# Kernel tuning notes

Hardware: AMD Instinct MI355X
Metric: run time of the kernel (lower is better)

Reference implementation:

```python
import jax, jax.numpy as jnp
import numpy as np

PAD = 20
MAX_DISP = 20
STRIDE2 = 2


def setup_inputs() -> dict:
    key = jax.random.key(0)
    k1, k2 = jax.random.split(key)
    B, C, H, W = 8, 256, 96, 128
    input1 = jax.random.normal(k1, (B, C, H, W), dtype=jnp.float32)
    input2 = jax.random.normal(k2, (B, C, H, W), dtype=jnp.float32)
    return {"input1": input1, "input2": input2}


def reference(input1, input2):
    B, C, H, W = input1.shape
    # zero-pad f2 spatially by PAD on all sides, as ZeroPad2d(pad_size)
    f2pad = jnp.pad(input2, ((0, 0), (0, 0), (PAD, PAD), (PAD, PAD)))
    # displacement offsets: range(i, i + 2*max_disp + 1, stride2) -> 21 per axis
    offs = jnp.arange(0, 2 * MAX_DISP + 1, STRIDE2)
    dy, dx = jnp.meshgrid(offs, offs, indexing="ij")  # h-major flatten matches torch flatten(-2,-1)
    dydx = jnp.stack([dy.ravel(), dx.ravel()], axis=-1)  # [441, 2]

    def step(_, d):
        # shifted view of f2pad: window element (dy, dx) for every pixel (i, j)
        win = jax.lax.dynamic_slice(f2pad, (0, 0, d[0], d[1]), (B, C, H, W))
        # per-pixel inner product over channels
        return None, jnp.einsum("bchw,bchw->bhw", input1, win)

    _, out = jax.lax.scan(step, None, dydx)  # [441, B, H, W]
    out = jnp.transpose(out, (1, 0, 2, 3))  # [B, 441, H, W]
    return out / C
```

## Files before the change

kernel.cpp:

```cpp
#include <hip/hip_runtime.h>
#include <hip/hip_bf16.h>


#define NB 8
#define NC 256
#define NH 96
#define NW 128
#define NU 64
#define ND 21
#define NK 441

typedef __attribute__((ext_vector_type(8))) short s16x8;
typedef __attribute__((ext_vector_type(4))) float f32x4;

__device__ __forceinline__ unsigned short f2bf(float f) {
    unsigned int x = __float_as_uint(f);
    x += 0x7fffu + ((x >> 16) & 1u);
    return (unsigned short)(x >> 16);
}

__global__ __launch_bounds__(256) void repack_kernel(
    const float* __restrict__ in1, const float* __restrict__ in2,
    unsigned short* __restrict__ xg, unsigned short* __restrict__ yg)
{
    int bid = blockIdx.x;
    int src = bid & 1;
    int ct  = (bid >> 1) & 3;
    int rest = bid >> 3;
    int i = rest % NH;
    int b = rest / NH;
    const float* in = src ? in2 : in1;
    unsigned short* og = src ? yg : xg;
    int c0 = ct * 64;

    __shared__ unsigned short tbuf[128][68];

    int tid = threadIdx.x;
    int j  = tid & 127;
    int ch = tid >> 7;
    #pragma unroll 4
    for (int p = 0; p < 32; ++p) {
        int cl = p * 2 + ch;
        float v = in[(((size_t)b * NC + (c0 + cl)) * NH + i) * NW + j];
        tbuf[j][cl] = f2bf(v);
    }
    __syncthreads();
    int c2 = tid & 31;
    int jr = tid >> 5;
    #pragma unroll
    for (int jj0 = 0; jj0 < 128; jj0 += 8) {
        int jj = jj0 + jr;
        int pj = jj & 1, u = jj >> 1;
        unsigned int val = *reinterpret_cast<const unsigned int*>(&tbuf[jj][2 * c2]);
        size_t o = ((((size_t)b * 2 + pj) * NH + i) * NU + u) * NC + c0 + 2 * c2;
        *reinterpret_cast<unsigned int*>(&og[o]) = val;
    }
}

#define XOFF 0
#define YOFF 65536
#define GOFF 131072
#define GPITCH 50
#define ZOFF (GOFF + 2 * 4 * 16 * GPITCH * 4)
#define LDSZ (ZOFF + 16)

__global__ __launch_bounds__(512) void corr_kernel(
    const unsigned short* __restrict__ xg,
    const unsigned short* __restrict__ yg,
    float* __restrict__ out)
{
    __shared__ __align__(16) unsigned char LDS[LDSZ];

    int bid = blockIdx.x;
    int i = bid % NH;
    int b = bid / NH;
    int tid = threadIdx.x;
    int lane = tid & 63;
    int wv = tid >> 6;
    int pj = wv >> 2;
    int tt = wv & 3;

    if (tid == 0) {
        uint4 z = {0u, 0u, 0u, 0u};
        *reinterpret_cast<uint4*>(&LDS[ZOFF]) = z;
    }

    {
        const uint4* src = reinterpret_cast<const uint4*>(xg);
        #pragma unroll
        for (int it = 0; it < 8; ++it) {
            int g = it * 512 + tid;
            int p = g >> 11;
            int rem = g & 2047;
            int u = rem >> 5, off = rem & 31;
            uint4 v = src[(((size_t)(b * 2 + p) * NH + i) * NU + u) * 32 + off];
            int lb = XOFF + (p << 15) + ((u * 512 + off * 16) ^ ((u & 7) << 4));
            *reinterpret_cast<uint4*>(&LDS[lb]) = v;
        }
    }

    const int m  = lane & 15;
    const int kq = lane >> 4;
    const int u  = tt * 16 + m;
    const int xrow = XOFF + (pj << 15) + u * 512;
    const int xsw  = (u & 7) << 4;

    int yb0, yb1, yb2, sw0, sw1, sw2;
    {
        int w0 = tt * 16 - 10 + m;
        int w1 = w0 + 16;
        int w2 = w0 + 32;
        yb0 = (w0 >= 0 && w0 < NU) ? (YOFF + (pj << 15) + w0 * 512) : -1;
        yb1 = (w1 >= 0 && w1 < NU) ? (YOFF + (pj << 15) + w1 * 512) : -1;
        yb2 = (w2 >= 0 && w2 < NU) ? (YOFF + (pj << 15) + w2 * 512) : -1;
        sw0 = (w0 & 7) << 4;
        sw1 = (w1 & 7) << 4;
        sw2 = (w2 & 7) << 4;
    }

    const float inv = 1.0f / 256.0f;

    for (int ky = 0; ky < ND; ++ky) {
        int r = i + 2 * ky - 20;
        bool valid = (r >= 0) && (r < NH);
        size_t obase = (((size_t)b * NK + 21 * ky) * NH + i) * NW + (tid & 127);

        if (valid) {
            const uint4* src = reinterpret_cast<const uint4*>(yg);
            #pragma unroll
            for (int it = 0; it < 8; ++it) {
                int g = it * 512 + tid;
                int p = g >> 11;
                int rem = g & 2047;
                int uu = rem >> 5, off = rem & 31;
                uint4 v = src[(((size_t)(b * 2 + p) * NH + r) * NU + uu) * 32 + off];
                int lb = YOFF + (p << 15) + ((uu * 512 + off * 16) ^ ((uu & 7) << 4));
                *reinterpret_cast<uint4*>(&LDS[lb]) = v;
            }
            __syncthreads();

            f32x4 acc0 = {0.f, 0.f, 0.f, 0.f};
            f32x4 acc1 = {0.f, 0.f, 0.f, 0.f};
            f32x4 acc2 = {0.f, 0.f, 0.f, 0.f};
            #pragma unroll
            for (int ks = 0; ks < 8; ++ks) {
                int c2 = (ks * 32 + kq * 8) * 2;
                s16x8 af = *reinterpret_cast<const s16x8*>(&LDS[xrow + (c2 ^ xsw)]);
                int a0 = (yb0 < 0) ? ZOFF : (yb0 + (c2 ^ sw0));
                s16x8 bf0 = *reinterpret_cast<const s16x8*>(&LDS[a0]);
                acc0 = __builtin_amdgcn_mfma_f32_16x16x32_bf16(af, bf0, acc0, 0, 0, 0);
                int a1 = (yb1 < 0) ? ZOFF : (yb1 + (c2 ^ sw1));
                s16x8 bf1 = *reinterpret_cast<const s16x8*>(&LDS[a1]);
                acc1 = __builtin_amdgcn_mfma_f32_16x16x32_bf16(af, bf1, acc1, 0, 0, 0);
                int a2 = (yb2 < 0) ? ZOFF : (yb2 + (c2 ^ sw2));
                s16x8 bf2 = *reinterpret_cast<const s16x8*>(&LDS[a2]);
                acc2 = __builtin_amdgcn_mfma_f32_16x16x32_bf16(af, bf2, acc2, 0, 0, 0);
            }

            int gb = GOFF + wv * (16 * GPITCH * 4);
            #pragma unroll
            for (int v4 = 0; v4 < 4; ++v4) {
                float* gr = reinterpret_cast<float*>(&LDS[gb + (kq * 4 + v4) * (GPITCH * 4)]);
                gr[m]      = acc0[v4];
                gr[16 + m] = acc1[v4];
                gr[32 + m] = acc2[v4];
            }
            __syncthreads();

            int j = tid & 127;
            int uo = j >> 1;
            int mo = uo & 15;
            const float* grow = reinterpret_cast<const float*>(
                &LDS[GOFF + (((j & 1) * 4 + (uo >> 4)) * 16 + mo) * (GPITCH * 4)]);
            for (int kx = tid >> 7; kx < ND; kx += 4) {
                out[obase + (size_t)kx * (NH * NW)] = grow[mo + kx] * inv;
            }
        } else {
            for (int kx = tid >> 7; kx < ND; kx += 4) {
                out[obase + (size_t)kx * (NH * NW)] = 0.0f;
            }
        }
    }
}

__global__ __launch_bounds__(256) void corr_naive(
    const float* __restrict__ in1, const float* __restrict__ in2, float* __restrict__ out)
{
    size_t o = (size_t)blockIdx.x * 256 + threadIdx.x;
    if (o >= (size_t)NB * NK * NH * NW) return;
    int j = o & 127;
    int i = (int)((o >> 7) % NH);
    size_t rest = o / ((size_t)NH * NW);
    int k = (int)(rest % NK);
    int b = (int)(rest / NK);
    int ky = k / ND, kx = k % ND;
    int r = i + 2 * ky - 20, jc = j + 2 * kx - 20;
    float s = 0.f;
    if (r >= 0 && r < NH && jc >= 0 && jc < NW) {
        const float* p1 = in1 + (((size_t)b * NC) * NH + i) * NW + j;
        const float* p2 = in2 + (((size_t)b * NC) * NH + r) * NW + jc;
        for (int c = 0; c < NC; ++c) { s += p1[0] * p2[0]; p1 += NH * NW; p2 += NH * NW; }
    }
    out[o] = s * (1.0f / 256.0f);
}

extern "C" void kernel_launch(void* const* d_in, const int* in_sizes, int n_in,
                              void* d_out, int out_size, void* d_ws, size_t ws_size,
                              hipStream_t stream) {
    const float* in1 = (const float*)d_in[0];
    const float* in2 = (const float*)d_in[1];
    float* out = (float*)d_out;

    const size_t elems_per_input = (size_t)NB * 2 * NH * NU * NC;
    const size_t need = 2 * elems_per_input * sizeof(unsigned short);

    if (ws_size < need) {
        size_t total = (size_t)NB * NK * NH * NW;
        corr_naive<<<(int)((total + 255) / 256), 256, 0, stream>>>(in1, in2, out);
        return;
    }

    unsigned short* xg = (unsigned short*)d_ws;
    unsigned short* yg = xg + elems_per_input;

    repack_kernel<<<NB * NH * 4 * 2, 256, 0, stream>>>(in1, in2, xg, yg);
    corr_kernel<<<NB * NH, 512, 0, stream>>>(xg, yg, out);
}
```

Before: 230.1 us.

## Load input1 directly into MFMA registers, use 32x32 MFMA, prefetch next row

The repack now covers only input2. The correlation kernel reads input1 straight from global memory, converts it to bf16, and holds it in registers as A fragments, which removes the xg workspace and its LDS staging. The compute moves to 32x32x16 MFMA tiles, and the next input2 row is loaded into registers while the current one is being computed, giving a double-buffered load. Fully padded rows are written as zeros up front, and the block-to-(b,i) mapping is reordered. The costs are higher register pressure (16 A fragments plus 8 staging vectors under launch_bounds 512,2) and strided fp32 reads of input1.

```diff
diff --git a/kernel.cpp b/kernel.cpp
--- a/kernel.cpp
+++ b/kernel.cpp
@@ -9,9 +9,10 @@
 #define NU 64
 #define ND 21
 #define NK 441
+#define HW (NH * NW)
 
 typedef __attribute__((ext_vector_type(8))) short s16x8;
-typedef __attribute__((ext_vector_type(4))) float f32x4;
+typedef __attribute__((ext_vector_type(16))) float f32x16;
 
 __device__ __forceinline__ unsigned short f2bf(float f) {
     unsigned int x = __float_as_uint(f);
@@ -19,30 +20,25 @@
     return (unsigned short)(x >> 16);
 }
 
-__global__ __launch_bounds__(256) void repack_kernel(
-    const float* __restrict__ in1, const float* __restrict__ in2,
-    unsigned short* __restrict__ xg, unsigned short* __restrict__ yg)
+__global__ __launch_bounds__(256) void repack3(
+    const float* __restrict__ in2, unsigned short* __restrict__ yg)
 {
     int bid = blockIdx.x;
-    int src = bid & 1;
-    int ct  = (bid >> 1) & 3;
-    int rest = bid >> 3;
-    int i = rest % NH;
+    int ct = bid & 3;
+    int rest = bid >> 2;
+    int r = rest % NH;
     int b = rest / NH;
-    const float* in = src ? in2 : in1;
-    unsigned short* og = src ? yg : xg;
     int c0 = ct * 64;
 
     __shared__ unsigned short tbuf[128][68];
 
     int tid = threadIdx.x;
-    int j  = tid & 127;
+    int j = tid & 127;
     int ch = tid >> 7;
     #pragma unroll 4
     for (int p = 0; p < 32; ++p) {
         int cl = p * 2 + ch;
-        float v = in[(((size_t)b * NC + (c0 + cl)) * NH + i) * NW + j];
-        tbuf[j][cl] = f2bf(v);
+        tbuf[j][cl] = f2bf(in2[(((size_t)b * NC + (c0 + cl)) * NH + r) * NW + j]);
     }
     __syncthreads();
     int c2 = tid & 31;
@@ -52,133 +48,148 @@
         int jj = jj0 + jr;
         int pj = jj & 1, u = jj >> 1;
         unsigned int val = *reinterpret_cast<const unsigned int*>(&tbuf[jj][2 * c2]);
-        size_t o = ((((size_t)b * 2 + pj) * NH + i) * NU + u) * NC + c0 + 2 * c2;
-        *reinterpret_cast<unsigned int*>(&og[o]) = val;
-    }
-}
-
-#define XOFF 0
-#define YOFF 65536
-#define GOFF 131072
-#define GPITCH 50
-#define ZOFF (GOFF + 2 * 4 * 16 * GPITCH * 4)
+        size_t o = ((((size_t)b * 2 + pj) * NH + r) * NU + u) * NC + c0 + 2 * c2;
+        *reinterpret_cast<unsigned int*>(&yg[o]) = val;
+    }
+}
+
+#define GOFF 65536
+#define GPITCH 55
+#define ZOFF (GOFF + 128 * GPITCH * 4)
 #define LDSZ (ZOFF + 16)
 
-__global__ __launch_bounds__(512) void corr_kernel(
-    const unsigned short* __restrict__ xg,
+__global__ __launch_bounds__(512, 2) void corr32r(
+    const float* __restrict__ in1,
     const unsigned short* __restrict__ yg,
     float* __restrict__ out)
 {
     __shared__ __align__(16) unsigned char LDS[LDSZ];
 
     int bid = blockIdx.x;
-    int i = bid % NH;
-    int b = bid / NH;
+    int b = bid & 7;
+    int i = bid >> 3;
     int tid = threadIdx.x;
     int lane = tid & 63;
     int wv = tid >> 6;
     int pj = wv >> 2;
-    int tt = wv & 3;
-
-    if (tid == 0) {
-        uint4 z = {0u, 0u, 0u, 0u};
-        *reinterpret_cast<uint4*>(&LDS[ZOFF]) = z;
-    }
-
-    {
-        const uint4* src = reinterpret_cast<const uint4*>(xg);
+    int ut = (wv >> 1) & 1;
+    int wt = wv & 1;
+    int l31 = lane & 31;
+    int hp = lane >> 5;
+
+    if (tid == 0) { *reinterpret_cast<uint4*>(&LDS[ZOFF]) = uint4{0u, 0u, 0u, 0u}; }
+
+    int ky0 = 21 - i; ky0 = (ky0 > 0) ? (ky0 >> 1) : 0;
+    int ky1 = (115 - i) >> 1; if (ky1 > 20) ky1 = 20;
+    int r0 = i + 2 * ky0 - 20;
+
+    const unsigned short* ygb = yg + (size_t)b * 2 * NH * NU * NC;
+
+    uint4 stg[8];
+    #pragma unroll
+    for (int m = 0; m < 8; ++m) {
+        int idx = m * 512 + tid;
+        int rho = idx >> 5, o32 = idx & 31;
+        int ps = rho >> 6, u = rho & 63;
+        stg[m] = *reinterpret_cast<const uint4*>(
+            ygb + ((size_t)ps * NH + r0) * (NU * NC) + u * NC + o32 * 8);
+    }
+
+    int u_a = ut * 32 + l31;
+    int j_a = 2 * u_a + pj;
+    const float* arow = in1 + (((size_t)b * NC) * NH + i) * NW + j_a;
+    s16x8 afr[16];
+    #pragma unroll
+    for (int ks = 0; ks < 16; ++ks) {
+        int c0 = ks * 16 + hp * 8;
+        s16x8 a;
         #pragma unroll
-        for (int it = 0; it < 8; ++it) {
-            int g = it * 512 + tid;
-            int p = g >> 11;
-            int rem = g & 2047;
-            int u = rem >> 5, off = rem & 31;
-            uint4 v = src[(((size_t)(b * 2 + p) * NH + i) * NU + u) * 32 + off];
-            int lb = XOFF + (p << 15) + ((u * 512 + off * 16) ^ ((u & 7) << 4));
-            *reinterpret_cast<uint4*>(&LDS[lb]) = v;
-        }
-    }
-
-    const int m  = lane & 15;
-    const int kq = lane >> 4;
-    const int u  = tt * 16 + m;
-    const int xrow = XOFF + (pj << 15) + u * 512;
-    const int xsw  = (u & 7) << 4;
-
-    int yb0, yb1, yb2, sw0, sw1, sw2;
-    {
-        int w0 = tt * 16 - 10 + m;
-        int w1 = w0 + 16;
-        int w2 = w0 + 32;
-        yb0 = (w0 >= 0 && w0 < NU) ? (YOFF + (pj << 15) + w0 * 512) : -1;
-        yb1 = (w1 >= 0 && w1 < NU) ? (YOFF + (pj << 15) + w1 * 512) : -1;
-        yb2 = (w2 >= 0 && w2 < NU) ? (YOFF + (pj << 15) + w2 * 512) : -1;
-        sw0 = (w0 & 7) << 4;
-        sw1 = (w1 & 7) << 4;
-        sw2 = (w2 & 7) << 4;
-    }
-
-    const float inv = 1.0f / 256.0f;
-
-    for (int ky = 0; ky < ND; ++ky) {
-        int r = i + 2 * ky - 20;
-        bool valid = (r >= 0) && (r < NH);
-        size_t obase = (((size_t)b * NK + 21 * ky) * NH + i) * NW + (tid & 127);
-
-        if (valid) {
-            const uint4* src = reinterpret_cast<const uint4*>(yg);
+        for (int s = 0; s < 8; ++s) a[s] = (short)f2bf(arow[(size_t)(c0 + s) * HW]);
+        afr[ks] = a;
+    }
+
+    #pragma unroll
+    for (int m = 0; m < 8; ++m) {
+        int idx = m * 512 + tid;
+        int rho = idx >> 5, o32 = idx & 31;
+        int u = rho & 63;
+        *reinterpret_cast<uint4*>(&LDS[rho * 512 + ((o32 * 16) ^ ((u & 7) << 4))]) = stg[m];
+    }
+
+    int jx = tid & 127;
+    int kq = tid >> 7;
+    for (int ky = 0; ky < ky0; ++ky) {
+        size_t ob = (((size_t)b * NK + 21 * ky) * NH + i) * NW + jx;
+        for (int kx = kq; kx < ND; kx += 4) out[ob + (size_t)kx * HW] = 0.0f;
+    }
+    for (int ky = ky1 + 1; ky <= 20; ++ky) {
+        size_t ob = (((size_t)b * NK + 21 * ky) * NH + i) * NW + jx;
+        for (int kx = kq; kx < ND; kx += 4) out[ob + (size_t)kx * HW] = 0.0f;
+    }
+
+    int w = ut * 32 - 10 + wt * 32 + l31;
+    bool bval = (w >= 0) && (w < NU);
+    int rowbase = (pj * 64 + w) * 512;
+    int wsw = (w & 7) << 4;
+
+    int ue = jx >> 1;
+    int gerow = ((jx & 1) * 2 + (ue >> 5)) * 32 + (ue & 31);
+    const int gebase = GOFF + (gerow * GPITCH + (ue & 31)) * 4;
+
+    int grow0 = (pj * 2 + ut) * 32;
+    int col = wt * 32 + l31;
+
+    for (int ky = ky0; ky <= ky1; ++ky) {
+        __syncthreads();
+
+        if (ky < ky1) {
+            int r2 = i + 2 * ky - 18;
             #pragma unroll
-            for (int it = 0; it < 8; ++it) {
-                int g = it * 512 + tid;
-                int p = g >> 11;
-                int rem = g & 2047;
-                int uu = rem >> 5, off = rem & 31;
-                uint4 v = src[(((size_t)(b * 2 + p) * NH + r) * NU + uu) * 32 + off];
-                int lb = YOFF + (p << 15) + ((uu * 512 + off * 16) ^ ((uu & 7) << 4));
-                *reinterpret_cast<uint4*>(&LDS[lb]) = v;
+            for (int m = 0; m < 8; ++m) {
+                int idx = m * 512 + tid;
+                int rho = idx >> 5, o32 = idx & 31;
+                int ps = rho >> 6, u = rho & 63;
+                stg[m] = *reinterpret_cast<const uint4*>(
+                    ygb + ((size_t)ps * NH + r2) * (NU * NC) + u * NC + o32 * 8);
             }
-            __syncthreads();
-
-            f32x4 acc0 = {0.f, 0.f, 0.f, 0.f};
-            f32x4 acc1 = {0.f, 0.f, 0.f, 0.f};
-            f32x4 acc2 = {0.f, 0.f, 0.f, 0.f};
+        }
+
+        f32x16 acc;
+        #pragma unroll
+        for (int z = 0; z < 16; ++z) acc[z] = 0.0f;
+        #pragma unroll
+        for (int k8 = 0; k8 < 16; ++k8) {
+            int off = k8 * 32 + hp * 16;
+            int a0 = bval ? (rowbase + (off ^ wsw)) : ZOFF;
+            s16x8 bf = *reinterpret_cast<const s16x8*>(&LDS[a0]);
+            acc = __builtin_amdgcn_mfma_f32_32x32x16_bf16(afr[k8], bf, acc, 0, 0, 0);
+        }
+
+        if (col < 52) {
             #pragma unroll
-            for (int ks = 0; ks < 8; ++ks) {
-                int c2 = (ks * 32 + kq * 8) * 2;
-                s16x8 af = *reinterpret_cast<const s16x8*>(&LDS[xrow + (c2 ^ xsw)]);
-                int a0 = (yb0 < 0) ? ZOFF : (yb0 + (c2 ^ sw0));
-                s16x8 bf0 = *reinterpret_cast<const s16x8*>(&LDS[a0]);
-                acc0 = __builtin_amdgcn_mfma_f32_16x16x32_bf16(af, bf0, acc0, 0, 0, 0);
-                int a1 = (yb1 < 0) ? ZOFF : (yb1 + (c2 ^ sw1));
-                s16x8 bf1 = *reinterpret_cast<const s16x8*>(&LDS[a1]);
-                acc1 = __builtin_amdgcn_mfma_f32_16x16x32_bf16(af, bf1, acc1, 0, 0, 0);
-                int a2 = (yb2 < 0) ? ZOFF : (yb2 + (c2 ^ sw2));
-                s16x8 bf2 = *reinterpret_cast<const s16x8*>(&LDS[a2]);
-                acc2 = __builtin_amdgcn_mfma_f32_16x16x32_bf16(af, bf2, acc2, 0, 0, 0);
+            for (int r16 = 0; r16 < 16; ++r16) {
+                int ur = (r16 & 3) + 8 * (r16 >> 2) + 4 * hp;
+                *reinterpret_cast<float*>(
+                    &LDS[GOFF + ((grow0 + ur) * GPITCH + col) * 4]) = acc[r16];
             }
-
-            int gb = GOFF + wv * (16 * GPITCH * 4);
+        }
+        __syncthreads();
+
+        if (ky < ky1) {
             #pragma unroll
-            for (int v4 = 0; v4 < 4; ++v4) {
-                float* gr = reinterpret_cast<float*>(&LDS[gb + (kq * 4 + v4) * (GPITCH * 4)]);
-                gr[m]      = acc0[v4];
-                gr[16 + m] = acc1[v4];
-                gr[32 + m] = acc2[v4];
+            for (int m = 0; m < 8; ++m) {
+                int idx = m * 512 + tid;
+                int rho = idx >> 5, o32 = idx & 31;
+                int u = rho & 63;
+                *reinterpret_cast<uint4*>(
+                    &LDS[rho * 512 + ((o32 * 16) ^ ((u & 7) << 4))]) = stg[m];
             }
-            __syncthreads();
-
-            int j = tid & 127;
-            int uo = j >> 1;
-            int mo = uo & 15;
-            const float* grow = reinterpret_cast<const float*>(
-                &LDS[GOFF + (((j & 1) * 4 + (uo >> 4)) * 16 + mo) * (GPITCH * 4)]);
-            for (int kx = tid >> 7; kx < ND; kx += 4) {
-                out[obase + (size_t)kx * (NH * NW)] = grow[mo + kx] * inv;
-            }
-        } else {
-            for (int kx = tid >> 7; kx < ND; kx += 4) {
-                out[obase + (size_t)kx * (NH * NW)] = 0.0f;
-            }
+        }
+
+        size_t ob = (((size_t)b * NK + 21 * ky) * NH + i) * NW + jx;
+        for (int kx = kq; kx < ND; kx += 4) {
+            out[ob + (size_t)kx * HW] =
+                *reinterpret_cast<const float*>(&LDS[gebase + kx * 4]) * 0.00390625f;
         }
     }
 }
@@ -211,8 +222,7 @@
     const float* in2 = (const float*)d_in[1];
     float* out = (float*)d_out;
 
-    const size_t elems_per_input = (size_t)NB * 2 * NH * NU * NC;
-    const size_t need = 2 * elems_per_input * sizeof(unsigned short);
+    const size_t need = (size_t)NB * 2 * NH * NU * NC * sizeof(unsigned short);
 
     if (ws_size < need) {
         size_t total = (size_t)NB * NK * NH * NW;
@@ -220,9 +230,8 @@
         return;
     }
 
-    unsigned short* xg = (unsigned short*)d_ws;
-    unsigned short* yg = xg + elems_per_input;
-
-    repack_kernel<<<NB * NH * 4 * 2, 256, 0, stream>>>(in1, in2, xg, yg);
-    corr_kernel<<<NB * NH, 512, 0, stream>>>(xg, yg, out);
-}
+    unsigned short* yg = (unsigned short*)d_ws;
+
+    repack3<<<NB * NH * 4, 256, 0, stream>>>(in2, yg);
+    corr32r<<<NB * NH, 512, 0, stream>>>(in1, yg, out);
+}
```

Result: slower. 333.1 us (+44.8%).
